# Kernel optimization log

Hardware: AMD Instinct MI355X
Metric: run time of the kernel (lower is better)

## Reference

```python
import jax, jax.numpy as jnp
import numpy as np

def setup_inputs() -> dict:
    key = jax.random.key(0)
    k1, k2, k3, k4, k5 = jax.random.split(key, 5)
    B, Lc, Lq, D = 32, 512, 64, 1024
    return {
        "c": jax.random.normal(k1, (B, Lc, D), dtype=jnp.float32),
        "q": jax.random.normal(k2, (B, Lq, D), dtype=jnp.float32),
        "proj_c": jax.random.normal(k3, (D, 1), dtype=jnp.float32) * 0.04,
        "proj_q": jax.random.normal(k4, (D, 1), dtype=jnp.float32) * 0.04,
        "proj_cq": jax.random.normal(k5, (1, 1, D), dtype=jnp.float32) * 0.04,
    }

def reference(c, q, proj_c, proj_q, proj_cq):
    # similarity: s0 + s1 + s2, shape [B, Lc, Lq]
    s0 = c @ proj_c                                   # [B, Lc, 1]
    s1 = jnp.swapaxes(q @ proj_q, 1, 2)               # [B, 1, Lq]
    s2 = jnp.einsum('bcd,bqd->bcq', c * proj_cq, q)   # [B, Lc, Lq]
    sim = s0 + s1 + s2

    # context-to-query attention
    a_c2q = jax.nn.softmax(sim, axis=-1)              # [B, Lc, Lq]
    c2q = jnp.einsum('bcq,bqd->bcd', a_c2q, q)        # [B, Lc, D]

    # query-to-context attention (max over query dim, softmax over context)
    a_q2c = jax.nn.softmax(jnp.max(sim, axis=-1), axis=-1)  # [B, Lc]
    q2c = jnp.einsum('bc,bcd->bd', a_q2c, c)[:, None, :]    # [B, 1, D], broadcasts over Lc

    out = jnp.concatenate((c, c2q, c * q2c, c * c2q), axis=-1)  # [B, Lc, 4D]
    return out
```

## Files before the change

kernel.cpp:

```cpp
#include <hip/hip_runtime.h>

#define B 32
#define LC 512
#define LQ 64
#define DD 1024


__global__ __launch_bounds__(256) void k0_s1(const float* __restrict__ q,
                                             const float* __restrict__ proj_q,
                                             float* __restrict__ s1) {
    int w = blockIdx.x * 4 + (threadIdx.x >> 6);
    int lane = threadIdx.x & 63;
    const float* qr = q + (size_t)w * DD;
    float acc = 0.f;
#pragma unroll
    for (int k = 0; k < 4; ++k) {
        int idx = k * 256 + lane * 4;
        float4 a = *(const float4*)(qr + idx);
        float4 p = *(const float4*)(proj_q + idx);
        acc += a.x * p.x + a.y * p.y + a.z * p.z + a.w * p.w;
    }
#pragma unroll
    for (int off = 32; off; off >>= 1) acc += __shfl_down(acc, off, 64);
    if (lane == 0) s1[w] = acc;
}

__global__ __launch_bounds__(128) void k1_sim(const float* __restrict__ c,
                                              const float* __restrict__ q,
                                              const float* __restrict__ proj_c,
                                              const float* __restrict__ proj_cq,
                                              const float* __restrict__ s1,
                                              float* __restrict__ sim,
                                              float* __restrict__ mfull) {
    const int b  = blockIdx.x >> 4;
    const int i0 = (blockIdx.x & 15) * 32;
    const int t  = threadIdx.x;

    __shared__ __align__(16) float cwT[64][36];
    __shared__ __align__(16) float qT[64][68];
    __shared__ float s0red[32][4];
    __shared__ float s0f[32];

    const int tx = t & 15;
    const int ty = t >> 4;

    float acc[4][4] = {{0.f}};
    float s0p = 0.f;

    const int crow  = t >> 2;
    const int ckoff = (t & 3) * 16;
    const float* cbase = c + ((size_t)(b * LC + i0 + crow)) * DD + ckoff;
    const int qrow  = t >> 1;
    const int qkoff = (t & 1) * 32;
    const float* qbase = q + ((size_t)(b * LQ + qrow)) * DD + qkoff;

    for (int k0 = 0; k0 < DD; k0 += 64) {
        __syncthreads();
#pragma unroll
        for (int m = 0; m < 4; ++m) {
            float4 cv = *(const float4*)(cbase + k0 + 4 * m);
            float4 pq = *(const float4*)(proj_cq + k0 + ckoff + 4 * m);
            float4 pc = *(const float4*)(proj_c + k0 + ckoff + 4 * m);
            s0p += cv.x * pc.x + cv.y * pc.y + cv.z * pc.z + cv.w * pc.w;
            cwT[ckoff + 4 * m + 0][crow] = cv.x * pq.x;
            cwT[ckoff + 4 * m + 1][crow] = cv.y * pq.y;
            cwT[ckoff + 4 * m + 2][crow] = cv.z * pq.z;
            cwT[ckoff + 4 * m + 3][crow] = cv.w * pq.w;
        }
#pragma unroll
        for (int m = 0; m < 8; ++m) {
            float4 qv = *(const float4*)(qbase + k0 + 4 * m);
            qT[qkoff + 4 * m + 0][qrow] = qv.x;
            qT[qkoff + 4 * m + 1][qrow] = qv.y;
            qT[qkoff + 4 * m + 2][qrow] = qv.z;
            qT[qkoff + 4 * m + 3][qrow] = qv.w;
        }
        __syncthreads();
#pragma unroll 8
        for (int kk = 0; kk < 64; ++kk) {
            float4 a4 = *(const float4*)&cwT[kk][ty * 4];
            float4 b4 = *(const float4*)&qT[kk][tx * 4];
            acc[0][0] += a4.x * b4.x; acc[0][1] += a4.x * b4.y; acc[0][2] += a4.x * b4.z; acc[0][3] += a4.x * b4.w;
            acc[1][0] += a4.y * b4.x; acc[1][1] += a4.y * b4.y; acc[1][2] += a4.y * b4.z; acc[1][3] += a4.y * b4.w;
            acc[2][0] += a4.z * b4.x; acc[2][1] += a4.z * b4.y; acc[2][2] += a4.z * b4.z; acc[2][3] += a4.z * b4.w;
            acc[3][0] += a4.w * b4.x; acc[3][1] += a4.w * b4.y; acc[3][2] += a4.w * b4.z; acc[3][3] += a4.w * b4.w;
        }
    }

    s0red[crow][t & 3] = s0p;
    __syncthreads();
    if (t < 32) s0f[t] = s0red[t][0] + s0red[t][1] + s0red[t][2] + s0red[t][3];
    __syncthreads();

    float4 s1v = *(const float4*)(s1 + b * LQ + tx * 4);
#pragma unroll
    for (int ii = 0; ii < 4; ++ii) {
        int r  = ty * 4 + ii;
        int ig = i0 + r;
        float v0 = acc[ii][0] + s1v.x;
        float v1 = acc[ii][1] + s1v.y;
        float v2 = acc[ii][2] + s1v.z;
        float v3 = acc[ii][3] + s1v.w;
        float rmax = fmaxf(fmaxf(v0, v1), fmaxf(v2, v3));
#pragma unroll
        for (int off = 1; off < 16; off <<= 1) rmax = fmaxf(rmax, __shfl_xor(rmax, off, 64));
        if (tx == 0) mfull[b * LC + ig] = rmax + s0f[r];
        float4 o = {v0, v1, v2, v3};
        *(float4*)(sim + ((size_t)(b * LC + ig)) * LQ + tx * 4) = o;
    }
}

__global__ __launch_bounds__(512) void k2b_aq2c(const float* __restrict__ mfull,
                                                float* __restrict__ aq2c) {
    int b = blockIdx.x;
    int t = threadIdx.x;
    float v = mfull[b * LC + t];
    __shared__ float redm[8];
    __shared__ float reds[8];
    float mx = v;
#pragma unroll
    for (int off = 32; off; off >>= 1) mx = fmaxf(mx, __shfl_xor(mx, off, 64));
    if ((t & 63) == 0) redm[t >> 6] = mx;
    __syncthreads();
    float bm = redm[0];
#pragma unroll
    for (int i = 1; i < 8; ++i) bm = fmaxf(bm, redm[i]);
    float e = __expf(v - bm);
    float s = e;
#pragma unroll
    for (int off = 32; off; off >>= 1) s += __shfl_xor(s, off, 64);
    if ((t & 63) == 0) reds[t >> 6] = s;
    __syncthreads();
    float bs = 0.f;
#pragma unroll
    for (int i = 0; i < 8; ++i) bs += reds[i];
    aq2c[b * LC + t] = e / bs;
}

__global__ __launch_bounds__(256) void k2c_q2c(const float* __restrict__ c,
                                               const float* __restrict__ aq2c,
                                               float* __restrict__ q2c) {
    int b  = blockIdx.x >> 3;
    int d0 = (blockIdx.x & 7) * 128;
    int t  = threadIdx.x;
    __shared__ float aL[LC];
    for (int i = t; i < LC; i += 256) aL[i] = aq2c[b * LC + i];
    __syncthreads();
    int tx = t & 31, ty = t >> 5;
    float4 acc = {0.f, 0.f, 0.f, 0.f};
    const float* cb = c + (size_t)b * LC * DD + d0 + tx * 4;
    for (int i = ty; i < LC; i += 8) {
        float a = aL[i];
        float4 cv = *(const float4*)(cb + (size_t)i * DD);
        acc.x += a * cv.x; acc.y += a * cv.y; acc.z += a * cv.z; acc.w += a * cv.w;
    }
    __shared__ __align__(16) float4 red[8][32];
    red[ty][tx] = acc;
    __syncthreads();
    if (t < 32) {
        float4 s = red[0][t];
#pragma unroll
        for (int k = 1; k < 8; ++k) {
            float4 v = red[k][t];
            s.x += v.x; s.y += v.y; s.z += v.z; s.w += v.w;
        }
        *(float4*)(q2c + b * DD + d0 + t * 4) = s;
    }
}

__global__ __launch_bounds__(256) void k3_out(const float* __restrict__ c,
                                              const float* __restrict__ q,
                                              const float* __restrict__ sim,
                                              const float* __restrict__ q2c,
                                              float* __restrict__ out) {
    int b  = blockIdx.x >> 4;
    int i0 = (blockIdx.x & 15) * 32;
    int t  = threadIdx.x;
    __shared__ __align__(16) float p[32][64];
    __shared__ __align__(16) float qc[64][128];

    int wave = t >> 6, lane = t & 63;
    for (int r = wave; r < 32; r += 4) {
        float v = sim[((size_t)(b * LC + i0 + r)) * LQ + lane];
        float mx = v;
#pragma unroll
        for (int off = 32; off; off >>= 1) mx = fmaxf(mx, __shfl_xor(mx, off, 64));
        float e = __expf(v - mx);
        float s = e;
#pragma unroll
        for (int off = 32; off; off >>= 1) s += __shfl_xor(s, off, 64);
        p[r][lane] = e / s;
    }

    int tx = t & 31;
    int ty = t >> 5;
    for (int d0 = 0; d0 < DD; d0 += 128) {
        __syncthreads();
#pragma unroll
        for (int k = 0; k < 8; ++k) {
            int j = ty + 8 * k;
            *(float4*)&qc[j][tx * 4] = *(const float4*)(q + ((size_t)(b * LQ + j)) * DD + d0 + tx * 4);
        }
        __syncthreads();
        float4 acc[4] = {{0.f,0.f,0.f,0.f},{0.f,0.f,0.f,0.f},{0.f,0.f,0.f,0.f},{0.f,0.f,0.f,0.f}};
#pragma unroll 8
        for (int j = 0; j < 64; ++j) {
            float4 q4 = *(const float4*)&qc[j][tx * 4];
#pragma unroll
            for (int k = 0; k < 4; ++k) {
                float pv = p[ty + 8 * k][j];
                acc[k].x += pv * q4.x; acc[k].y += pv * q4.y;
                acc[k].z += pv * q4.z; acc[k].w += pv * q4.w;
            }
        }
        float4 g2 = *(const float4*)(q2c + b * DD + d0 + tx * 4);
#pragma unroll
        for (int k = 0; k < 4; ++k) {
            int i = i0 + ty + 8 * k;
            float4 cv = *(const float4*)(c + ((size_t)(b * LC + i)) * DD + d0 + tx * 4);
            float* ob = out + ((size_t)(b * LC + i)) * (4 * DD) + d0 + tx * 4;
            *(float4*)(ob) = cv;
            *(float4*)(ob + DD) = acc[k];
            float4 t2 = {cv.x * g2.x, cv.y * g2.y, cv.z * g2.z, cv.w * g2.w};
            *(float4*)(ob + 2 * DD) = t2;
            float4 t3 = {cv.x * acc[k].x, cv.y * acc[k].y, cv.z * acc[k].z, cv.w * acc[k].w};
            *(float4*)(ob + 3 * DD) = t3;
        }
    }
}

extern "C" void kernel_launch(void* const* d_in, const int* in_sizes, int n_in,
                              void* d_out, int out_size, void* d_ws, size_t ws_size,
                              hipStream_t stream) {
    const float* c       = (const float*)d_in[0];
    const float* q       = (const float*)d_in[1];
    const float* proj_c  = (const float*)d_in[2];
    const float* proj_q  = (const float*)d_in[3];
    const float* proj_cq = (const float*)d_in[4];
    float* out = (float*)d_out;
    float* ws  = (float*)d_ws;

    float* s1    = ws;
    float* mfull = ws + 2048;
    float* aq2c  = ws + 18432;
    float* q2c   = ws + 34816;
    float* sim   = ws + 67584;

    hipLaunchKernelGGL(k0_s1,   dim3(512), dim3(256), 0, stream, q, proj_q, s1);
    hipLaunchKernelGGL(k1_sim,  dim3(512), dim3(128), 0, stream, c, q, proj_c, proj_cq, s1, sim, mfull);
    hipLaunchKernelGGL(k2b_aq2c,dim3(32),  dim3(512), 0, stream, mfull, aq2c);
    hipLaunchKernelGGL(k2c_q2c, dim3(256), dim3(256), 0, stream, c, aq2c, q2c);
    hipLaunchKernelGGL(k3_out,  dim3(512), dim3(256), 0, stream, c, q, sim, q2c, out);
}
```

Before: 432.5 us.

## Use bf16 MFMA for similarity and attention matmuls with register prefetch

Rewrites the similarity GEMM kernel and the output kernel to convert operands to bf16 and run them on the matrix cores with 16x16x32 bf16 MFMA instructions instead of scalar FP32 FMA loops. Both kernels now prefetch the next k-chunk into registers while the current chunk is processed, and the similarity kernel moves from 128 to 256 threads per block. This removes the ALU-bound FP32 inner loops, but rounding c*proj_cq, q and the softmax probabilities to bf16 loses precision. Output writes, which are the dominant memory traffic, stay the same.

```diff
diff --git a/kernel.cpp b/kernel.cpp
--- a/kernel.cpp
+++ b/kernel.cpp
@@ -5,6 +5,22 @@
 #define LQ 64
 #define DD 1024
 
+
+typedef __attribute__((ext_vector_type(8))) short bf16x8;
+typedef __attribute__((ext_vector_type(4))) float f32x4;
+
+__device__ inline short f2bf(float f) {
+    unsigned u = __builtin_bit_cast(unsigned, f);
+    u += 0x7FFFu + ((u >> 16) & 1u);
+    return (short)(u >> 16);
+}
+
+__device__ inline bf16x8 pack8(float4 a, float4 b) {
+    bf16x8 r;
+    r[0] = f2bf(a.x); r[1] = f2bf(a.y); r[2] = f2bf(a.z); r[3] = f2bf(a.w);
+    r[4] = f2bf(b.x); r[5] = f2bf(b.y); r[6] = f2bf(b.z); r[7] = f2bf(b.w);
+    return r;
+}
 
 __global__ __launch_bounds__(256) void k0_s1(const float* __restrict__ q,
                                              const float* __restrict__ proj_q,
@@ -25,7 +41,7 @@
     if (lane == 0) s1[w] = acc;
 }
 
-__global__ __launch_bounds__(128) void k1_sim(const float* __restrict__ c,
+__global__ __launch_bounds__(256) void k1_sim(const float* __restrict__ c,
                                               const float* __restrict__ q,
                                               const float* __restrict__ proj_c,
                                               const float* __restrict__ proj_cq,
@@ -35,78 +51,94 @@
     const int b  = blockIdx.x >> 4;
     const int i0 = (blockIdx.x & 15) * 32;
     const int t  = threadIdx.x;
-
-    __shared__ __align__(16) float cwT[64][36];
-    __shared__ __align__(16) float qT[64][68];
-    __shared__ float s0red[32][4];
-    __shared__ float s0f[32];
-
-    const int tx = t & 15;
-    const int ty = t >> 4;
-
-    float acc[4][4] = {{0.f}};
+    const int w  = t >> 6, lane = t & 63;
+    const int l15 = lane & 15, quad = lane >> 4;
+
+    __shared__ __align__(16) short sA[32][72];
+    __shared__ __align__(16) short sB[64][72];
+    __shared__ float rmaxL[32][4];
+    __shared__ float s0red[32][8];
+
+    const int arow = t >> 3, ag = t & 7;
+    const int brow = t >> 2, bg = t & 3;
+
+    const float* cbase = c + (size_t)(b * LC + i0 + arow) * DD + ag * 8;
+    const float* qbase = q + (size_t)(b * LQ + brow) * DD + bg * 16;
+
+    f32x4 acc[2] = {{0.f,0.f,0.f,0.f},{0.f,0.f,0.f,0.f}};
     float s0p = 0.f;
 
-    const int crow  = t >> 2;
-    const int ckoff = (t & 3) * 16;
-    const float* cbase = c + ((size_t)(b * LC + i0 + crow)) * DD + ckoff;
-    const int qrow  = t >> 1;
-    const int qkoff = (t & 1) * 32;
-    const float* qbase = q + ((size_t)(b * LQ + qrow)) * DD + qkoff;
-
-    for (int k0 = 0; k0 < DD; k0 += 64) {
+    float4 a0 = *(const float4*)(cbase + 0);
+    float4 a1 = *(const float4*)(cbase + 4);
+    float4 b0 = *(const float4*)(qbase + 0);
+    float4 b1 = *(const float4*)(qbase + 4);
+    float4 b2 = *(const float4*)(qbase + 8);
+    float4 b3 = *(const float4*)(qbase + 12);
+
+    for (int kc = 0; kc < 16; ++kc) {
+        float4 na0, na1, nb0, nb1, nb2, nb3;
+        if (kc < 15) {
+            const float* cn = cbase + (kc + 1) * 64;
+            const float* qn = qbase + (kc + 1) * 64;
+            na0 = *(const float4*)(cn + 0);
+            na1 = *(const float4*)(cn + 4);
+            nb0 = *(const float4*)(qn + 0);
+            nb1 = *(const float4*)(qn + 4);
+            nb2 = *(const float4*)(qn + 8);
+            nb3 = *(const float4*)(qn + 12);
+        }
+        {
+            const float* pcq = proj_cq + kc * 64 + ag * 8;
+            const float* pc  = proj_c  + kc * 64 + ag * 8;
+            float4 p0 = *(const float4*)(pcq + 0);
+            float4 p1 = *(const float4*)(pcq + 4);
+            float4 c0 = *(const float4*)(pc + 0);
+            float4 c1 = *(const float4*)(pc + 4);
+            s0p += a0.x * c0.x + a0.y * c0.y + a0.z * c0.z + a0.w * c0.w
+                 + a1.x * c1.x + a1.y * c1.y + a1.z * c1.z + a1.w * c1.w;
+            float4 m0 = {a0.x * p0.x, a0.y * p0.y, a0.z * p0.z, a0.w * p0.w};
+            float4 m1 = {a1.x * p1.x, a1.y * p1.y, a1.z * p1.z, a1.w * p1.w};
+            *(bf16x8*)&sA[arow][ag * 8] = pack8(m0, m1);
+            *(bf16x8*)&sB[brow][bg * 16 + 0] = pack8(b0, b1);
+            *(bf16x8*)&sB[brow][bg * 16 + 8] = pack8(b2, b3);
+        }
         __syncthreads();
 #pragma unroll
-        for (int m = 0; m < 4; ++m) {
-            float4 cv = *(const float4*)(cbase + k0 + 4 * m);
-            float4 pq = *(const float4*)(proj_cq + k0 + ckoff + 4 * m);
-            float4 pc = *(const float4*)(proj_c + k0 + ckoff + 4 * m);
-            s0p += cv.x * pc.x + cv.y * pc.y + cv.z * pc.z + cv.w * pc.w;
-            cwT[ckoff + 4 * m + 0][crow] = cv.x * pq.x;
-            cwT[ckoff + 4 * m + 1][crow] = cv.y * pq.y;
-            cwT[ckoff + 4 * m + 2][crow] = cv.z * pq.z;
-            cwT[ckoff + 4 * m + 3][crow] = cv.w * pq.w;
-        }
-#pragma unroll
-        for (int m = 0; m < 8; ++m) {
-            float4 qv = *(const float4*)(qbase + k0 + 4 * m);
-            qT[qkoff + 4 * m + 0][qrow] = qv.x;
-            qT[qkoff + 4 * m + 1][qrow] = qv.y;
-            qT[qkoff + 4 * m + 2][qrow] = qv.z;
-            qT[qkoff + 4 * m + 3][qrow] = qv.w;
+        for (int s = 0; s < 2; ++s) {
+            int ko = s * 32 + quad * 8;
+            bf16x8 bf = *(const bf16x8*)&sB[w * 16 + l15][ko];
+#pragma unroll
+            for (int mt = 0; mt < 2; ++mt) {
+                bf16x8 af = *(const bf16x8*)&sA[mt * 16 + l15][ko];
+                acc[mt] = __builtin_amdgcn_mfma_f32_16x16x32_bf16(af, bf, acc[mt], 0, 0, 0);
+            }
         }
         __syncthreads();
-#pragma unroll 8
-        for (int kk = 0; kk < 64; ++kk) {
-            float4 a4 = *(const float4*)&cwT[kk][ty * 4];
-            float4 b4 = *(const float4*)&qT[kk][tx * 4];
-            acc[0][0] += a4.x * b4.x; acc[0][1] += a4.x * b4.y; acc[0][2] += a4.x * b4.z; acc[0][3] += a4.x * b4.w;
-            acc[1][0] += a4.y * b4.x; acc[1][1] += a4.y * b4.y; acc[1][2] += a4.y * b4.z; acc[1][3] += a4.y * b4.w;
-            acc[2][0] += a4.z * b4.x; acc[2][1] += a4.z * b4.y; acc[2][2] += a4.z * b4.z; acc[2][3] += a4.z * b4.w;
-            acc[3][0] += a4.w * b4.x; acc[3][1] += a4.w * b4.y; acc[3][2] += a4.w * b4.z; acc[3][3] += a4.w * b4.w;
-        }
-    }
-
-    s0red[crow][t & 3] = s0p;
-    __syncthreads();
-    if (t < 32) s0f[t] = s0red[t][0] + s0red[t][1] + s0red[t][2] + s0red[t][3];
-    __syncthreads();
-
-    float4 s1v = *(const float4*)(s1 + b * LQ + tx * 4);
-#pragma unroll
-    for (int ii = 0; ii < 4; ++ii) {
-        int r  = ty * 4 + ii;
-        int ig = i0 + r;
-        float v0 = acc[ii][0] + s1v.x;
-        float v1 = acc[ii][1] + s1v.y;
-        float v2 = acc[ii][2] + s1v.z;
-        float v3 = acc[ii][3] + s1v.w;
-        float rmax = fmaxf(fmaxf(v0, v1), fmaxf(v2, v3));
-#pragma unroll
-        for (int off = 1; off < 16; off <<= 1) rmax = fmaxf(rmax, __shfl_xor(rmax, off, 64));
-        if (tx == 0) mfull[b * LC + ig] = rmax + s0f[r];
-        float4 o = {v0, v1, v2, v3};
-        *(float4*)(sim + ((size_t)(b * LC + ig)) * LQ + tx * 4) = o;
+        if (kc < 15) { a0 = na0; a1 = na1; b0 = nb0; b1 = nb1; b2 = nb2; b3 = nb3; }
+    }
+
+    s0red[arow][ag] = s0p;
+    float s1j = s1[b * LQ + w * 16 + l15];
+#pragma unroll
+    for (int mt = 0; mt < 2; ++mt) {
+#pragma unroll
+        for (int r = 0; r < 4; ++r) {
+            float v = acc[mt][r] + s1j;
+            int ig = i0 + mt * 16 + quad * 4 + r;
+            sim[(size_t)(b * LC + ig) * LQ + w * 16 + l15] = v;
+            float rm = v;
+#pragma unroll
+            for (int off = 1; off < 16; off <<= 1) rm = fmaxf(rm, __shfl_xor(rm, off, 16));
+            if (l15 == 0) rmaxL[mt * 16 + quad * 4 + r][w] = rm;
+        }
+    }
+    __syncthreads();
+    if (t < 32) {
+        float s0v = 0.f;
+#pragma unroll
+        for (int k = 0; k < 8; ++k) s0v += s0red[t][k];
+        float mm = fmaxf(fmaxf(rmaxL[t][0], rmaxL[t][1]), fmaxf(rmaxL[t][2], rmaxL[t][3]));
+        mfull[b * LC + i0 + t] = mm + s0v;
     }
 }
 
@@ -173,59 +205,100 @@
                                               const float* __restrict__ sim,
                                               const float* __restrict__ q2c,
                                               float* __restrict__ out) {
-    int b  = blockIdx.x >> 4;
-    int i0 = (blockIdx.x & 15) * 32;
-    int t  = threadIdx.x;
-    __shared__ __align__(16) float p[32][64];
-    __shared__ __align__(16) float qc[64][128];
-
-    int wave = t >> 6, lane = t & 63;
-    for (int r = wave; r < 32; r += 4) {
-        float v = sim[((size_t)(b * LC + i0 + r)) * LQ + lane];
+    const int b  = blockIdx.x >> 4;
+    const int i0 = (blockIdx.x & 15) * 32;
+    const int t  = threadIdx.x;
+    const int w  = t >> 6, lane = t & 63;
+    const int l15 = lane & 15, quad = lane >> 4;
+
+    __shared__ __align__(16) short pA[32][72];
+    __shared__ __align__(16) short sBq[64][72];
+    __shared__ __align__(16) float ct[32][68];
+
+#pragma unroll
+    for (int rr = 0; rr < 8; ++rr) {
+        int row = w * 8 + rr;
+        float v = sim[(size_t)(b * LC + i0 + row) * LQ + lane];
         float mx = v;
 #pragma unroll
         for (int off = 32; off; off >>= 1) mx = fmaxf(mx, __shfl_xor(mx, off, 64));
         float e = __expf(v - mx);
-        float s = e;
-#pragma unroll
-        for (int off = 32; off; off >>= 1) s += __shfl_xor(s, off, 64);
-        p[r][lane] = e / s;
-    }
-
-    int tx = t & 31;
-    int ty = t >> 5;
-    for (int d0 = 0; d0 < DD; d0 += 128) {
+        float ss = e;
+#pragma unroll
+        for (int off = 32; off; off >>= 1) ss += __shfl_xor(ss, off, 64);
+        pA[row][lane] = f2bf(e / ss);
+    }
+
+    const int j0 = (t & 31) * 2, dg = t >> 5;
+    const int erow = t >> 4, ed = (t & 15) * 4;
+
+    const float* qb0 = q + (size_t)(b * LQ + j0) * DD + dg * 8;
+    const float* qb1 = qb0 + DD;
+
+    float4 r0 = *(const float4*)(qb0 + 0);
+    float4 r1 = *(const float4*)(qb0 + 4);
+    float4 r2 = *(const float4*)(qb1 + 0);
+    float4 r3 = *(const float4*)(qb1 + 4);
+
+    for (int dc = 0; dc < 16; ++dc) {
+        const int d0 = dc * 64;
+        float4 n0, n1, n2, n3;
+        if (dc < 15) {
+            n0 = *(const float4*)(qb0 + (dc + 1) * 64);
+            n1 = *(const float4*)(qb0 + (dc + 1) * 64 + 4);
+            n2 = *(const float4*)(qb1 + (dc + 1) * 64);
+            n3 = *(const float4*)(qb1 + (dc + 1) * 64 + 4);
+        }
+        float4 cc0 = *(const float4*)(c + (size_t)(b * LC + i0 + erow) * DD + d0 + ed);
+        float4 cc1 = *(const float4*)(c + (size_t)(b * LC + i0 + erow + 16) * DD + d0 + ed);
+        float4 g2  = *(const float4*)(q2c + b * DD + d0 + ed);
+
+        const float* fr0 = (const float*)&r0;
+        const float* fr1 = (const float*)&r1;
+        const float* fr2 = (const float*)&r2;
+        const float* fr3 = (const float*)&r3;
+#pragma unroll
+        for (int e = 0; e < 8; ++e) {
+            float v0 = (e < 4) ? fr0[e] : fr1[e - 4];
+            float v1 = (e < 4) ? fr2[e] : fr3[e - 4];
+            unsigned pk = (unsigned)(unsigned short)f2bf(v0)
+                        | ((unsigned)(unsigned short)f2bf(v1) << 16);
+            *(unsigned*)&sBq[dg * 8 + e][j0] = pk;
+        }
         __syncthreads();
-#pragma unroll
-        for (int k = 0; k < 8; ++k) {
-            int j = ty + 8 * k;
-            *(float4*)&qc[j][tx * 4] = *(const float4*)(q + ((size_t)(b * LQ + j)) * DD + d0 + tx * 4);
-        }
+
+        f32x4 acc[2] = {{0.f,0.f,0.f,0.f},{0.f,0.f,0.f,0.f}};
+#pragma unroll
+        for (int s = 0; s < 2; ++s) {
+            int ko = s * 32 + quad * 8;
+            bf16x8 bf = *(const bf16x8*)&sBq[w * 16 + l15][ko];
+#pragma unroll
+            for (int mt = 0; mt < 2; ++mt) {
+                bf16x8 af = *(const bf16x8*)&pA[mt * 16 + l15][ko];
+                acc[mt] = __builtin_amdgcn_mfma_f32_16x16x32_bf16(af, bf, acc[mt], 0, 0, 0);
+            }
+        }
+#pragma unroll
+        for (int mt = 0; mt < 2; ++mt)
+#pragma unroll
+            for (int r = 0; r < 4; ++r)
+                ct[mt * 16 + quad * 4 + r][w * 16 + l15] = acc[mt][r];
         __syncthreads();
-        float4 acc[4] = {{0.f,0.f,0.f,0.f},{0.f,0.f,0.f,0.f},{0.f,0.f,0.f,0.f},{0.f,0.f,0.f,0.f}};
-#pragma unroll 8
-        for (int j = 0; j < 64; ++j) {
-            float4 q4 = *(const float4*)&qc[j][tx * 4];
-#pragma unroll
-            for (int k = 0; k < 4; ++k) {
-                float pv = p[ty + 8 * k][j];
-                acc[k].x += pv * q4.x; acc[k].y += pv * q4.y;
-                acc[k].z += pv * q4.z; acc[k].w += pv * q4.w;
-            }
-        }
-        float4 g2 = *(const float4*)(q2c + b * DD + d0 + tx * 4);
-#pragma unroll
-        for (int k = 0; k < 4; ++k) {
-            int i = i0 + ty + 8 * k;
-            float4 cv = *(const float4*)(c + ((size_t)(b * LC + i)) * DD + d0 + tx * 4);
-            float* ob = out + ((size_t)(b * LC + i)) * (4 * DD) + d0 + tx * 4;
-            *(float4*)(ob) = cv;
-            *(float4*)(ob + DD) = acc[k];
-            float4 t2 = {cv.x * g2.x, cv.y * g2.y, cv.z * g2.z, cv.w * g2.w};
-            *(float4*)(ob + 2 * DD) = t2;
-            float4 t3 = {cv.x * acc[k].x, cv.y * acc[k].y, cv.z * acc[k].z, cv.w * acc[k].w};
-            *(float4*)(ob + 3 * DD) = t3;
-        }
+
+#pragma unroll
+        for (int k = 0; k < 2; ++k) {
+            int row = erow + 16 * k;
+            float4 cc = k ? cc1 : cc0;
+            float4 cqv = *(const float4*)&ct[row][ed];
+            float* ob = out + (size_t)(b * LC + i0 + row) * (4 * DD) + d0 + ed;
+            *(float4*)(ob) = cc;
+            *(float4*)(ob + DD) = cqv;
+            float4 o2 = {cc.x * g2.x, cc.y * g2.y, cc.z * g2.z, cc.w * g2.w};
+            *(float4*)(ob + 2 * DD) = o2;
+            float4 o3 = {cc.x * cqv.x, cc.y * cqv.y, cc.z * cqv.z, cc.w * cqv.w};
+            *(float4*)(ob + 3 * DD) = o3;
+        }
+        if (dc < 15) { r0 = n0; r1 = n1; r2 = n2; r3 = n3; }
     }
 }
 
@@ -246,9 +319,9 @@
     float* q2c   = ws + 34816;
     float* sim   = ws + 67584;
 
-    hipLaunchKernelGGL(k0_s1,   dim3(512), dim3(256), 0, stream, q, proj_q, s1);
-    hipLaunchKernelGGL(k1_sim,  dim3(512), dim3(128), 0, stream, c, q, proj_c, proj_cq, s1, sim, mfull);
-    hipLaunchKernelGGL(k2b_aq2c,dim3(32),  dim3(512), 0, stream, mfull, aq2c);
-    hipLaunchKernelGGL(k2c_q2c, dim3(256), dim3(256), 0, stream, c, aq2c, q2c);
-    hipLaunchKernelGGL(k3_out,  dim3(512), dim3(256), 0, stream, c, q, sim, q2c, out);
-}
+    hipLaunchKernelGGL(k0_s1,    dim3(512), dim3(256), 0, stream, q, proj_q, s1);
+    hipLaunchKernelGGL(k1_sim,   dim3(512), dim3(256), 0, stream, c, q, proj_c, proj_cq, s1, sim, mfull);
+    hipLaunchKernelGGL(k2b_aq2c, dim3(32),  dim3(512), 0, stream, mfull, aq2c);
+    hipLaunchKernelGGL(k2c_q2c,  dim3(256), dim3(256), 0, stream, c, aq2c, q2c);
+    hipLaunchKernelGGL(k3_out,   dim3(512), dim3(256), 0, stream, c, q, sim, q2c, out);
+}
```

Result: faster. 390.6 us (-9.7%).
